# Kernel tuning notes

Hardware: AMD Instinct MI355X
Metric: run time of the kernel (lower is better)

The kernel has to match this reference:

```python
import jax, jax.numpy as jnp
import numpy as np

NUM_ENTITIES = 100000
BATCH_SIZE = 4096
E_STATIC = 250000
E_NEW = 4096
D_ENT = 128
D_REL = 64
N_REL = 9
N_TYPES = 3
N_INTENTS = 8
NUM_LAYERS = 3
SCALE = 0.05


def _make_edges(key, n):
    ks = jax.random.split(key, 5)
    src = jax.random.randint(ks[0], (n,), 0, NUM_ENTITIES, dtype=jnp.int32)
    st = jax.random.randint(ks[1], (n,), 0, N_TYPES, dtype=jnp.int32)
    tgt = jax.random.randint(ks[2], (n,), 0, NUM_ENTITIES, dtype=jnp.int32)
    tt = jax.random.randint(ks[3], (n,), 0, N_TYPES, dtype=jnp.int32)
    rel = jax.random.randint(ks[4], (n,), 0, N_REL, dtype=jnp.int32)
    return jnp.stack([src, st, tgt, tt, rel], axis=1)


def setup_inputs() -> dict:
    key = jax.random.key(0)
    ks = jax.random.split(key, 16)
    return {
        'new_edges': _make_edges(ks[0], E_NEW),
        'new_node_types': jax.random.randint(ks[1], (BATCH_SIZE,), 0, N_TYPES, dtype=jnp.int32),
        'static_edges': _make_edges(ks[2], E_STATIC),
        'entity_embeddings': SCALE * jax.random.normal(ks[3], (NUM_ENTITIES - BATCH_SIZE, D_ENT), jnp.float32),
        'default_emb': SCALE * jax.random.normal(ks[4], (N_TYPES, D_ENT), jnp.float32),
        'relation_emb': SCALE * jax.random.normal(ks[5], (N_REL, D_REL), jnp.float32),
        'W_rel': SCALE * jax.random.normal(ks[6], (N_REL, D_ENT, D_REL), jnp.float32),
        'b_rel': SCALE * jax.random.normal(ks[7], (N_REL, D_REL), jnp.float32),
        'W_msg': SCALE * jax.random.normal(ks[8], (N_REL, D_ENT, D_ENT), jnp.float32),
        'W_intent': SCALE * jax.random.normal(ks[9], (N_TYPES, D_ENT, N_INTENTS), jnp.float32),
        'b_intent': SCALE * jax.random.normal(ks[10], (N_TYPES, N_INTENTS), jnp.float32),
        'W_ibn': SCALE * jax.random.normal(ks[11], (N_TYPES, N_INTENTS, N_REL), jnp.float32),
        'b_ibn': SCALE * jax.random.normal(ks[12], (N_TYPES, N_REL), jnp.float32),
    }


def multi_dense(lookups, values, W, b=None, act=None):
    # Same math as tf.gather(W, lookups) followed by values @ w, but computed
    # against all D (<=9) weight slices then selected, to avoid materializing
    # a [E, d_in, d_out] gathered-weights tensor.
    out_all = jnp.einsum('ei,dio->edo', values, W)  # [E, D, d_out]
    out = jnp.take_along_axis(out_all, lookups[:, None, None], axis=1)[:, 0]
    if b is not None:
        out = out + b[lookups]
    return act(out) if act is not None else out


def reference(new_edges, new_node_types, static_edges, entity_embeddings,
              default_emb, relation_emb, W_rel, b_rel, W_msg,
              W_intent, b_intent, W_ibn, b_ibn):
    edges = jnp.concatenate([new_edges, static_edges], axis=0)  # [E, 5]
    sources = edges[:, 0]
    targets = edges[:, 2]
    target_types = edges[:, 3]
    relations = edges[:, 4]

    rel_e = relation_emb[relations]  # [E, D_REL]
    # first BATCH_SIZE entity slots come from type default embeddings
    ent = jnp.concatenate([default_emb[new_node_types], entity_embeddings], axis=0)  # [N, D_ENT]

    layer_edge_weights = []
    for _ in range(NUM_LAYERS):
        src = ent[sources]  # [E, D_ENT]
        tgt = ent[targets]  # [E, D_ENT]
        # per-target intent distribution and per-relation intent weights
        intents = multi_dense(target_types, tgt, W_intent, b_intent, jax.nn.softmax)  # [E, N_INTENTS]
        rel_w = multi_dense(target_types, intents, W_ibn, b_ibn, jax.nn.softmax)  # [E, N_REL]
        iw = jnp.take_along_axis(rel_w, relations[:, None], axis=1)[:, 0]  # [E]
        # per-relation transform of source embeddings
        src_rel = multi_dense(relations, src, W_rel, b_rel, jax.nn.selu)  # [E, D_REL]
        scores = jnp.einsum('er,er,e->e', src_rel, rel_e, iw)  # [E]
        exp_s = jnp.exp(scores)
        denom = jax.ops.segment_sum(exp_s, targets, num_segments=NUM_ENTITIES)  # [N]
        # tf.math.reciprocal_no_nan semantics
        safe = jnp.where(denom != 0, denom, 1.0)
        recip = jnp.where(denom != 0, 1.0 / safe, 0.0)
        dist = exp_s * recip[targets]  # scatter-softmax over incoming edges
        # inference: dropout is identity
        msg = dist[:, None] * multi_dense(relations, src, W_msg, None, None)  # [E, D_ENT]
        ent = jax.ops.segment_sum(msg, targets, num_segments=NUM_ENTITIES)  # [N, D_ENT]
        layer_edge_weights.append(dist)

    return ent, jnp.stack(layer_edge_weights)  # [N, D_ENT], [L, E]
```

## Files before the change

### kernel.cpp

```cpp
#include <hip/hip_runtime.h>
#include <cstddef>
#include <cstdint>

#define NE 100000
#define EN 4096
#define ET 254096
#define D 128
#define DR 64
#define NR 9
#define NT 3
#define NI 8
#define TE 256
#define TILES_X 28

using frag  = __attribute__((ext_vector_type(8))) short;
using f32x4 = __attribute__((ext_vector_type(4))) float;

__device__ __forceinline__ ushort f2b(float x) {
  union { float f; uint32_t u; } v; v.f = x;
  uint32_t r = v.u + 0x7FFFu + ((v.u >> 16) & 1u);
  return (ushort)(r >> 16);
}

__device__ __forceinline__ uint32_t cvtpk(float lo, float hi) {
  uint32_t r;
  asm("v_cvt_pk_bf16_f32 %0, %1, %2" : "=v"(r) : "v"(lo), "v"(hi));
  return r;
}

__device__ __forceinline__ frag lds_rd(const ushort* b, int row, int k) {
  const int ch = ((k >> 3) ^ (row & 7));
  return *(const frag*)(b + row * D + (ch << 3));
}
__device__ __forceinline__ void lds_wr(ushort* b, int row, int ch, frag v) {
  *(frag*)(b + row * D + ((ch ^ (row & 7)) << 3)) = v;
}
__device__ __forceinline__ void lds_wr2(ushort* b, int row, int k, uint32_t v) {
  const int ch = (k >> 3) ^ (row & 7);
  *(uint32_t*)(b + row * D + (ch << 3) + (k & 7)) = v;
}

__global__ void k_init(ushort* __restrict__ entb, const int* __restrict__ ntypes,
                       const float* __restrict__ def, const float* __restrict__ emb) {
  int i = blockIdx.x * blockDim.x + threadIdx.x;
  if (i >= NE * (D / 4)) return;
  int row = i >> 5, ch = i & 31;
  float4 v;
  if (row < EN) v = ((const float4*)(def + ntypes[row] * D))[ch];
  else v = ((const float4*)(emb + (size_t)(row - EN) * D))[ch];
  ushort4 h;
  h.x = f2b(v.x); h.y = f2b(v.y); h.z = f2b(v.z); h.w = f2b(v.w);
  ((ushort4*)entb)[i] = h;
}

__global__ void k_zero_cnt(int* cnt) { if (threadIdx.x < 48) cnt[threadIdx.x] = 0; }

__global__ __launch_bounds__(256) void k_hist2(const int* __restrict__ nedg,
                                               const int* __restrict__ sedg,
                                               int* __restrict__ cnt,
                                               int* __restrict__ thist) {
  __shared__ int h[NR];
  if (threadIdx.x < NR) h[threadIdx.x] = 0;
  __syncthreads();
  int e = blockIdx.x * 256 + threadIdx.x;
  if (e < ET) {
    const int* p = (e < EN) ? nedg + (size_t)e * 5 : sedg + (size_t)(e - EN) * 5;
    atomicAdd(&h[p[4]], 1);
    atomicAdd(&thist[p[2]], 1);
  }
  __syncthreads();
  if (threadIdx.x < NR && h[threadIdx.x]) atomicAdd(&cnt[threadIdx.x], h[threadIdx.x]);
}

__global__ void k_prefix(const int* __restrict__ cnt, int* __restrict__ base,
                         int* __restrict__ head) {
  if (threadIdx.x == 0) {
    int acc = 0;
    for (int r = 0; r < NR; r++) { base[r] = acc; head[r] = acc; acc += cnt[r]; }
  }
}

__global__ __launch_bounds__(256) void k_scan1(const int* __restrict__ hist,
                                               int* __restrict__ local_ex,
                                               int* __restrict__ bsum, int n) {
  __shared__ int s[256];
  int i = blockIdx.x * 256 + threadIdx.x;
  int v = (i < n) ? hist[i] : 0;
  s[threadIdx.x] = v;
  __syncthreads();
  for (int off = 1; off < 256; off <<= 1) {
    int t = (threadIdx.x >= off) ? s[threadIdx.x - off] : 0;
    __syncthreads();
    s[threadIdx.x] += t;
    __syncthreads();
  }
  if (i < n) local_ex[i] = s[threadIdx.x] - v;
  if (threadIdx.x == 255) bsum[blockIdx.x] = s[255];
}

__global__ __launch_bounds__(512) void k_scan2(int* __restrict__ bsum, int nb) {
  __shared__ int s[512];
  int v = (threadIdx.x < nb) ? bsum[threadIdx.x] : 0;
  s[threadIdx.x] = v;
  __syncthreads();
  for (int off = 1; off < 512; off <<= 1) {
    int t = (threadIdx.x >= off) ? s[threadIdx.x - off] : 0;
    __syncthreads();
    s[threadIdx.x] += t;
    __syncthreads();
  }
  if (threadIdx.x < nb) bsum[threadIdx.x] = s[threadIdx.x] - v;
}

__global__ void k_scan3(int* __restrict__ tgt_off, const int* __restrict__ bsum,
                        int* __restrict__ thead) {
  int i = blockIdx.x * 256 + threadIdx.x;
  if (i < NE) {
    int v = tgt_off[i] + bsum[i >> 8];
    tgt_off[i] = v;
    thead[i] = v;
  }
  if (i == 0) tgt_off[NE] = ET;
}

__global__ __launch_bounds__(256) void k_scatter3(const int* __restrict__ nedg,
                                                  const int* __restrict__ sedg,
                                                  int* __restrict__ head,
                                                  int* __restrict__ thead,
                                                  int* __restrict__ bucket,
                                                  int* __restrict__ tpos,
                                                  int* __restrict__ esorted) {
  __shared__ int h[NR], bb[NR];
  if (threadIdx.x < NR) h[threadIdx.x] = 0;
  __syncthreads();
  int e = blockIdx.x * 256 + threadIdx.x;
  int r = -1, pos = 0, t = 0;
  if (e < ET) {
    const int* p = (e < EN) ? nedg + (size_t)e * 5 : sedg + (size_t)(e - EN) * 5;
    r = p[4]; t = p[2];
    pos = atomicAdd(&h[r], 1);
  }
  __syncthreads();
  if (threadIdx.x < NR)
    bb[threadIdx.x] = h[threadIdx.x] ? atomicAdd(&head[threadIdx.x], h[threadIdx.x]) : 0;
  __syncthreads();
  if (r >= 0) {
    bucket[bb[r] + pos] = e;
    int pt = atomicAdd(&thead[t], 1);
    tpos[e] = pt;
    esorted[pt] = e;
  }
}

__global__ __launch_bounds__(1024) void k_iw(
    const ushort* __restrict__ entb,
    const float* __restrict__ W_int, const float* __restrict__ b_int,
    const float* __restrict__ W_ibn, const float* __restrict__ b_ibn,
    float* __restrict__ IW) {
  __shared__ ushort sE[TE * D];
  __shared__ ushort sWi[NT * 16 * D];
  __shared__ float sInt3[TE * 25];
  __shared__ float sbint[NT * NI], sWibn[NT * NI * NR], sbibn[NT * NR];

  const int tid = threadIdx.x;
  const int lane = tid & 63, wv = tid >> 6, g = lane >> 4, c = lane & 15;

  {
    float a[2], b[2];
#pragma unroll
    for (int j = 0; j < 2; j++) {
      int i = tid + j * 1024;
      if (i < NT * NI * (D / 2)) {
        int tt = i / (NI * D / 2), rem = i % (NI * D / 2), jj = rem / (D / 2), k2 = rem % (D / 2);
        const float* Wi = W_int + (size_t)tt * D * NI;
        a[j] = Wi[(2 * k2) * NI + jj]; b[j] = Wi[(2 * k2 + 1) * NI + jj];
      }
    }
#pragma unroll
    for (int j = 0; j < 2; j++) {
      int i = tid + j * 1024;
      if (i < NT * NI * (D / 2)) {
        int tt = i / (NI * D / 2), rem = i % (NI * D / 2), jj = rem / (D / 2), k2 = rem % (D / 2);
        lds_wr2(sWi, tt * 16 + jj, 2 * k2, cvtpk(a[j], b[j]));
      }
    }
  }
  for (int i = tid; i < NT * 8 * (D / 2); i += 1024) {
    int tt = i / (8 * D / 2), rem = i % (8 * D / 2), j = rem / (D / 2), k2 = rem % (D / 2);
    lds_wr2(sWi, tt * 16 + 8 + j, 2 * k2, 0u);
  }
  if (tid < NT * NI) sbint[tid] = b_int[tid];
  for (int i = tid; i < NT * NI * NR; i += 1024) sWibn[i] = W_ibn[i];
  if (tid < NT * NR) sbibn[tid] = b_ibn[tid];

  const int ebase = blockIdx.x * TE;
  const int nrow = min(TE, NE - ebase);
  {
    frag tmp[4];
#pragma unroll
    for (int j = 0; j < 4; j++) {
      int i = tid + j * 1024, row = i >> 4, ch = i & 15;
      tmp[j] = (row < nrow) ? ((const frag*)(entb + (size_t)(ebase + row) * D))[ch] : (frag){};
    }
#pragma unroll
    for (int j = 0; j < 4; j++) {
      int i = tid + j * 1024, row = i >> 4, ch = i & 15;
      lds_wr(sE, row, ch, tmp[j]);
    }
  }
  __syncthreads();

  {
    f32x4 accI[NT];
#pragma unroll
    for (int tt = 0; tt < NT; tt++) accI[tt] = (f32x4){0.f, 0.f, 0.f, 0.f};
#pragma unroll
    for (int ks = 0; ks < 4; ks++) {
      const int k = ks * 32 + g * 8;
      frag a = lds_rd(sE, wv * 16 + c, k);
#pragma unroll
      for (int tt = 0; tt < NT; tt++) {
        frag b = lds_rd(sWi, tt * 16 + c, k);
        accI[tt] = __builtin_amdgcn_mfma_f32_16x16x32_bf16(a, b, accI[tt], 0, 0, 0);
      }
    }
    if (c < NI) {
      const int rb = wv * 16 + g * 4;
#pragma unroll
      for (int tt = 0; tt < NT; tt++)
#pragma unroll
        for (int q = 0; q < 4; q++) sInt3[(rb + q) * 25 + tt * 8 + c] = accI[tt][q];
    }
  }
  __syncthreads();

  float* stg = (float*)sE;
  {
    const int row = tid & 255, tt = tid >> 8;
    if (tt < NT && row < nrow) {
      float it[NI], mx = -1e30f;
#pragma unroll
      for (int j = 0; j < NI; j++) {
        it[j] = sInt3[row * 25 + tt * 8 + j] + sbint[tt * NI + j];
        mx = fmaxf(mx, it[j]);
      }
      float ssum = 0.f;
#pragma unroll
      for (int j = 0; j < NI; j++) { it[j] = __expf(it[j] - mx); ssum += it[j]; }
      const float inv = 1.f / ssum;
      float qv[NR];
#pragma unroll
      for (int k = 0; k < NR; k++) qv[k] = sbibn[tt * NR + k];
#pragma unroll
      for (int j = 0; j < NI; j++) {
        const float ij = it[j] * inv;
#pragma unroll
        for (int k = 0; k < NR; k++) qv[k] = fmaf(ij, sWibn[(tt * NI + j) * NR + k], qv[k]);
      }
      float m9 = qv[0];
#pragma unroll
      for (int k = 1; k < NR; k++) m9 = fmaxf(m9, qv[k]);
      float s9 = 0.f;
#pragma unroll
      for (int k = 0; k < NR; k++) s9 += __expf(qv[k] - m9);
      const float i9 = 1.f / s9;
#pragma unroll
      for (int k = 0; k < NR; k++) stg[row * 27 + tt * 9 + k] = __expf(qv[k] - m9) * i9;
    }
  }
  __syncthreads();

  const int n27 = nrow * 27;
  float* outp = IW + (size_t)ebase * 27;
  for (int i = tid; i < n27; i += 1024) outp[i] = stg[i];
}

__global__ __launch_bounds__(1024) void k_pass1(
    const ushort* __restrict__ entb,
    const int* __restrict__ nedg, const int* __restrict__ sedg,
    const int* __restrict__ cnt, const int* __restrict__ base_g,
    const int* __restrict__ bucket, const int* __restrict__ tpos,
    const float* __restrict__ IW,
    const float* __restrict__ rel_emb,
    const float* __restrict__ W_rel, const float* __restrict__ b_rel,
    const float* __restrict__ W_msg,
    ushort* __restrict__ msgbuf, float* __restrict__ exps_s) {
  const int r = blockIdx.y;
  __shared__ ushort sA[TE * D];
  __shared__ ushort sWm[D * D];
  __shared__ ushort sWr[DR * D];
  __shared__ int sTP[TE];
  __shared__ float sIW[TE];
  __shared__ float sbrel[DR], srele[DR];

  const int tid = threadIdx.x;
  const int lane = tid & 63;
  const int wv = tid >> 6;
  const int g = lane >> 4;
  const int c = lane & 15;

  {
    const float* Wr = W_rel + (size_t)r * D * DR;
    const float* Wm = W_msg + (size_t)r * D * D;
    float ra[4], rb[4], ma[8], mb[8];
#pragma unroll
    for (int j = 0; j < 4; j++) {
      int i = tid + j * 1024, k2 = i / DR, n = i % DR;
      ra[j] = Wr[(2 * k2) * DR + n]; rb[j] = Wr[(2 * k2 + 1) * DR + n];
    }
#pragma unroll
    for (int j = 0; j < 8; j++) {
      int i = tid + j * 1024, k2 = i >> 7, n = i & 127;
      ma[j] = Wm[(2 * k2) * D + n]; mb[j] = Wm[(2 * k2 + 1) * D + n];
    }
#pragma unroll
    for (int j = 0; j < 4; j++) {
      int i = tid + j * 1024, k2 = i / DR, n = i % DR;
      lds_wr2(sWr, n, 2 * k2, cvtpk(ra[j], rb[j]));
    }
#pragma unroll
    for (int j = 0; j < 8; j++) {
      int i = tid + j * 1024, k2 = i >> 7, n = i & 127;
      lds_wr2(sWm, n, 2 * k2, cvtpk(ma[j], mb[j]));
    }
  }
  if (tid < DR) { sbrel[tid] = b_rel[r * DR + tid]; srele[tid] = rel_emb[r * DR + tid]; }

  const int nr = cnt[r];
  const int bbase = base_g[r];
  const int ntiles = (nr + TE - 1) / TE;

  for (int tile = blockIdx.x; tile < ntiles; tile += gridDim.x) {
    const int e0 = tile * TE;
    const int ne = min(TE, nr - e0);
    __syncthreads();

    {
      const int row = tid & 255, h = tid >> 8;
      int eg = 0;
      if (row < ne) eg = bucket[bbase + e0 + row];
      const int* p = (eg < EN) ? nedg + (size_t)eg * 5 : sedg + (size_t)(eg - EN) * 5;
      const int s = p[0];
      if (h == 0 && row < ne) {
        const int t = p[2], tt = p[3];
        sTP[row] = tpos[eg];
        sIW[row] = IW[((size_t)t * NT + tt) * NR + r];
      }
      const frag* rp = (const frag*)(entb + (size_t)s * D);
      frag tmp[4];
#pragma unroll
      for (int j = 0; j < 4; j++) tmp[j] = rp[h * 4 + j];
#pragma unroll
      for (int j = 0; j < 4; j++) lds_wr(sA, row, h * 4 + j, tmp[j]);
    }
    __syncthreads();

    f32x4 accR[4], accM[8];
#pragma unroll
    for (int nt = 0; nt < 4; nt++) accR[nt] = (f32x4){0.f, 0.f, 0.f, 0.f};
#pragma unroll
    for (int nt = 0; nt < 8; nt++) accM[nt] = (f32x4){0.f, 0.f, 0.f, 0.f};
#pragma unroll
    for (int ks = 0; ks < 4; ks++) {
      const int k = ks * 32 + g * 8;
      frag a0 = lds_rd(sA, wv * 16 + c, k);
#pragma unroll
      for (int nt = 0; nt < 4; nt++) {
        frag b = lds_rd(sWr, nt * 16 + c, k);
        accR[nt] = __builtin_amdgcn_mfma_f32_16x16x32_bf16(a0, b, accR[nt], 0, 0, 0);
      }
#pragma unroll
      for (int nt = 0; nt < 8; nt++) {
        frag b = lds_rd(sWm, nt * 16 + c, k);
        accM[nt] = __builtin_amdgcn_mfma_f32_16x16x32_bf16(a0, b, accM[nt], 0, 0, 0);
      }
    }

    const int mb = wv * 16 + g * 4;

    float es[4];
    {
      float v[4] = {0.f, 0.f, 0.f, 0.f};
#pragma unroll
      for (int nt = 0; nt < 4; nt++) {
        const int col = nt * 16 + c;
        const float br = sbrel[col], re = srele[col];
#pragma unroll
        for (int q = 0; q < 4; q++) {
          const float x = accR[nt][q] + br;
          const float sl = x > 0.f ? 1.0507009873554805f * x
                                   : 1.7580993408473766f * (__expf(x) - 1.f);
          v[q] = fmaf(sl, re, v[q]);
        }
      }
#pragma unroll
      for (int off = 1; off < 16; off <<= 1)
#pragma unroll
        for (int q = 0; q < 4; q++) v[q] += __shfl_xor(v[q], off, 64);
#pragma unroll
      for (int q = 0; q < 4; q++) {
        const int m = mb + q;
        es[q] = __expf(v[q] * sIW[m]);
        if (c == 0 && m < ne) exps_s[sTP[m]] = es[q];
      }
    }

    {
#pragma unroll
      for (int q = 0; q < 4; q++) {
        const int m = mb + q;
        ushort* mrow = msgbuf + (size_t)sTP[m] * D;
#pragma unroll
        for (int nt = 0; nt < 8; nt++) {
          float val = accM[nt][q] * es[q];
          float other = __shfl_xor(val, 1, 64);
          if (!(c & 1) && m < ne)
            *(uint32_t*)(mrow + nt * 16 + c) = cvtpk(val, other);
        }
      }
    }
  }
}

__global__ __launch_bounds__(256) void k_agg(
    const ushort* __restrict__ msgbuf, const float* __restrict__ exps_s,
    const int* __restrict__ tgt_off, const int* __restrict__ esorted,
    ushort* __restrict__ entb, float* __restrict__ fout,
    float* __restrict__ dout, int last) {
  const int lg = threadIdx.x & 15;
  const int grp = threadIdx.x >> 4;
  const int ngrp = gridDim.x * 16;
  for (int t = blockIdx.x * 16 + grp; t < NE; t += ngrp) {
    const int beg = tgt_off[t], end = tgt_off[t + 1];
    float a[8] = {0.f, 0.f, 0.f, 0.f, 0.f, 0.f, 0.f, 0.f};
    float dsum = 0.f;
    for (int j = beg; j < end; j++) {
      const uint4 pk = *(const uint4*)(msgbuf + (size_t)j * D + lg * 8);
      dsum += exps_s[j];
      a[0] += __uint_as_float(pk.x << 16); a[1] += __uint_as_float(pk.x & 0xFFFF0000u);
      a[2] += __uint_as_float(pk.y << 16); a[3] += __uint_as_float(pk.y & 0xFFFF0000u);
      a[4] += __uint_as_float(pk.z << 16); a[5] += __uint_as_float(pk.z & 0xFFFF0000u);
      a[6] += __uint_as_float(pk.w << 16); a[7] += __uint_as_float(pk.w & 0xFFFF0000u);
    }
    const float rec = (dsum != 0.f) ? 1.f / dsum : 0.f;
#pragma unroll
    for (int i = 0; i < 8; i++) a[i] *= rec;
    if (last) {
      float4* o = (float4*)(fout + (size_t)t * D + lg * 8);
      o[0] = make_float4(a[0], a[1], a[2], a[3]);
      o[1] = make_float4(a[4], a[5], a[6], a[7]);
    } else {
      uint4 pk;
      pk.x = (uint32_t)f2b(a[0]) | ((uint32_t)f2b(a[1]) << 16);
      pk.y = (uint32_t)f2b(a[2]) | ((uint32_t)f2b(a[3]) << 16);
      pk.z = (uint32_t)f2b(a[4]) | ((uint32_t)f2b(a[5]) << 16);
      pk.w = (uint32_t)f2b(a[6]) | ((uint32_t)f2b(a[7]) << 16);
      *(uint4*)(entb + (size_t)t * D + lg * 8) = pk;
    }
    for (int j = beg + lg; j < end; j += 16) dout[esorted[j]] = exps_s[j] * rec;
  }
}

extern "C" void kernel_launch(void* const* d_in, const int* in_sizes, int n_in,
                              void* d_out, int out_size, void* d_ws, size_t ws_size,
                              hipStream_t stream) {
  const int* nedg = (const int*)d_in[0];
  const int* ntypes = (const int*)d_in[1];
  const int* sedg = (const int*)d_in[2];
  const float* emb = (const float*)d_in[3];
  const float* def = (const float*)d_in[4];
  const float* rel_emb = (const float*)d_in[5];
  const float* W_rel = (const float*)d_in[6];
  const float* b_rel = (const float*)d_in[7];
  const float* W_msg = (const float*)d_in[8];
  const float* W_int = (const float*)d_in[9];
  const float* b_int = (const float*)d_in[10];
  const float* W_ibn = (const float*)d_in[11];
  const float* b_ibn = (const float*)d_in[12];
  float* out = (float*)d_out;

  char* w = (char*)d_ws;
  size_t off = 0;
  ushort* entb = (ushort*)(w + off); off += (size_t)NE * D * 2;
  ushort* msgbuf = (ushort*)(w + off); off += (size_t)ET * D * 2;
  float* exps_s = (float*)(w + off); off += (size_t)ET * 4;
  int* bucket = (int*)(w + off); off += (size_t)ET * 4;
  int* tpos = (int*)(w + off); off += (size_t)ET * 4;
  int* esorted = (int*)(w + off); off += (size_t)ET * 4;
  int* tgt_off = (int*)(w + off); off += (size_t)(NE + 4) * 4;
  int* thead = (int*)(w + off); off += (size_t)NE * 4;
  int* thist = (int*)(w + off); off += (size_t)NE * 4;
  int* bsum = (int*)(w + off); off += 2048;
  int* cnt = (int*)(w + off); off += 192;
  float* IW = (float*)(w + off); off += (size_t)NE * NT * NR * 4;
  int* base_g = cnt + 16;
  int* head = cnt + 32;
  float* dist_base = out + (size_t)NE * D;

  const int eblocks = (ET + 255) / 256;
  const int nb = (NE + 255) / 256;

  k_init<<<dim3((NE * (D / 4) + 255) / 256), 256, 0, stream>>>(entb, ntypes, def, emb);
  k_zero_cnt<<<1, 64, 0, stream>>>(cnt);
  hipMemsetAsync(thist, 0, (size_t)NE * 4, stream);
  k_hist2<<<dim3(eblocks), 256, 0, stream>>>(nedg, sedg, cnt, thist);
  k_prefix<<<1, 64, 0, stream>>>(cnt, base_g, head);
  k_scan1<<<dim3(nb), 256, 0, stream>>>(thist, tgt_off, bsum, NE);
  k_scan2<<<1, 512, 0, stream>>>(bsum, nb);
  k_scan3<<<dim3(nb), 256, 0, stream>>>(tgt_off, bsum, thead);
  k_scatter3<<<dim3(eblocks), 256, 0, stream>>>(nedg, sedg, head, thead, bucket, tpos,
                                                esorted);

  for (int l = 0; l < 3; l++) {
    k_iw<<<dim3(nb), 1024, 0, stream>>>(entb, W_int, b_int, W_ibn, b_ibn, IW);
    k_pass1<<<dim3(TILES_X, NR), 1024, 0, stream>>>(
        entb, nedg, sedg, cnt, base_g, bucket, tpos, IW, rel_emb, W_rel, b_rel, W_msg,
        msgbuf, exps_s);
    k_agg<<<dim3(2048), 256, 0, stream>>>(msgbuf, exps_s, tgt_off, esorted, entb, out,
                                          dist_base + (size_t)l * ET, l == 2);
  }
}
```

Baseline: 357.1 us.

## Halve pass1 edge tile, cache W_rel fragments in registers, run two blocks/CU

Shrinks the per-relation edge tile in k_pass1 from 256 to 128 rows and the block from 1024 to 512 threads, with launch bounds asking for two blocks per CU. The W_rel tile is staged through the sA buffer once and then held in registers as MFMA B fragments, which drops the sWr LDS array and its repeated LDS reads in the inner loop. The lower LDS footprint is meant to let two blocks share a CU, so one block's gather and load phases can overlap the other's MFMA work. The cost is more register pressure from the 16 cached fragments and a doubled tile count per relation. k_iw is changed to hard-code 256 rows so it keeps its old tiling.

```diff
diff --git a/kernel.cpp b/kernel.cpp
--- a/kernel.cpp
+++ b/kernel.cpp
@@ -10,8 +10,8 @@
 #define NR 9
 #define NT 3
 #define NI 8
-#define TE 256
-#define TILES_X 28
+#define TE 128
+#define TILES_X 56
 
 using frag  = __attribute__((ext_vector_type(8))) short;
 using f32x4 = __attribute__((ext_vector_type(4))) float;
@@ -157,9 +157,9 @@
     const float* __restrict__ W_int, const float* __restrict__ b_int,
     const float* __restrict__ W_ibn, const float* __restrict__ b_ibn,
     float* __restrict__ IW) {
-  __shared__ ushort sE[TE * D];
+  __shared__ ushort sE[256 * D];
   __shared__ ushort sWi[NT * 16 * D];
-  __shared__ float sInt3[TE * 25];
+  __shared__ float sInt3[256 * 25];
   __shared__ float sbint[NT * NI], sWibn[NT * NI * NR], sbibn[NT * NR];
 
   const int tid = threadIdx.x;
@@ -193,8 +193,8 @@
   for (int i = tid; i < NT * NI * NR; i += 1024) sWibn[i] = W_ibn[i];
   if (tid < NT * NR) sbibn[tid] = b_ibn[tid];
 
-  const int ebase = blockIdx.x * TE;
-  const int nrow = min(TE, NE - ebase);
+  const int ebase = blockIdx.x * 256;
+  const int nrow = min(256, NE - ebase);
   {
     frag tmp[4];
 #pragma unroll
@@ -275,7 +275,7 @@
   for (int i = tid; i < n27; i += 1024) outp[i] = stg[i];
 }
 
-__global__ __launch_bounds__(1024) void k_pass1(
+__global__ __launch_bounds__(512, 2) void k_pass1(
     const ushort* __restrict__ entb,
     const int* __restrict__ nedg, const int* __restrict__ sedg,
     const int* __restrict__ cnt, const int* __restrict__ base_g,
@@ -288,7 +288,6 @@
   const int r = blockIdx.y;
   __shared__ ushort sA[TE * D];
   __shared__ ushort sWm[D * D];
-  __shared__ ushort sWr[DR * D];
   __shared__ int sTP[TE];
   __shared__ float sIW[TE];
   __shared__ float sbrel[DR], srele[DR];
@@ -302,29 +301,24 @@
   {
     const float* Wr = W_rel + (size_t)r * D * DR;
     const float* Wm = W_msg + (size_t)r * D * D;
-    float ra[4], rb[4], ma[8], mb[8];
-#pragma unroll
-    for (int j = 0; j < 4; j++) {
-      int i = tid + j * 1024, k2 = i / DR, n = i % DR;
-      ra[j] = Wr[(2 * k2) * DR + n]; rb[j] = Wr[(2 * k2 + 1) * DR + n];
-    }
-#pragma unroll
-    for (int j = 0; j < 8; j++) {
-      int i = tid + j * 1024, k2 = i >> 7, n = i & 127;
-      ma[j] = Wm[(2 * k2) * D + n]; mb[j] = Wm[(2 * k2 + 1) * D + n];
-    }
-#pragma unroll
-    for (int j = 0; j < 4; j++) {
-      int i = tid + j * 1024, k2 = i / DR, n = i % DR;
-      lds_wr2(sWr, n, 2 * k2, cvtpk(ra[j], rb[j]));
-    }
-#pragma unroll
-    for (int j = 0; j < 8; j++) {
-      int i = tid + j * 1024, k2 = i >> 7, n = i & 127;
-      lds_wr2(sWm, n, 2 * k2, cvtpk(ma[j], mb[j]));
+    for (int i = tid; i < (D / 2) * DR; i += 512) {
+      int k2 = i / DR, n = i % DR;
+      lds_wr2(sA, n, 2 * k2, cvtpk(Wr[(2 * k2) * DR + n], Wr[(2 * k2 + 1) * DR + n]));
+    }
+    for (int i = tid; i < (D / 2) * D; i += 512) {
+      int k2 = i >> 7, n = i & 127;
+      lds_wr2(sWm, n, 2 * k2, cvtpk(Wm[(2 * k2) * D + n], Wm[(2 * k2 + 1) * D + n]));
     }
   }
   if (tid < DR) { sbrel[tid] = b_rel[r * DR + tid]; srele[tid] = rel_emb[r * DR + tid]; }
+  __syncthreads();
+
+  frag bR[4][4];
+#pragma unroll
+  for (int nt = 0; nt < 4; nt++)
+#pragma unroll
+    for (int ks = 0; ks < 4; ks++)
+      bR[nt][ks] = lds_rd(sA, nt * 16 + c, ks * 32 + g * 8);
 
   const int nr = cnt[r];
   const int bbase = base_g[r];
@@ -336,7 +330,7 @@
     __syncthreads();
 
     {
-      const int row = tid & 255, h = tid >> 8;
+      const int row = tid & 127, h = tid >> 7;
       int eg = 0;
       if (row < ne) eg = bucket[bbase + e0 + row];
       const int* p = (eg < EN) ? nedg + (size_t)eg * 5 : sedg + (size_t)(eg - EN) * 5;
@@ -365,10 +359,8 @@
       const int k = ks * 32 + g * 8;
       frag a0 = lds_rd(sA, wv * 16 + c, k);
 #pragma unroll
-      for (int nt = 0; nt < 4; nt++) {
-        frag b = lds_rd(sWr, nt * 16 + c, k);
-        accR[nt] = __builtin_amdgcn_mfma_f32_16x16x32_bf16(a0, b, accR[nt], 0, 0, 0);
-      }
+      for (int nt = 0; nt < 4; nt++)
+        accR[nt] = __builtin_amdgcn_mfma_f32_16x16x32_bf16(a0, bR[nt][ks], accR[nt], 0, 0, 0);
 #pragma unroll
       for (int nt = 0; nt < 8; nt++) {
         frag b = lds_rd(sWm, nt * 16 + c, k);
@@ -513,7 +505,7 @@
 
   for (int l = 0; l < 3; l++) {
     k_iw<<<dim3(nb), 1024, 0, stream>>>(entb, W_int, b_int, W_ibn, b_ibn, IW);
-    k_pass1<<<dim3(TILES_X, NR), 1024, 0, stream>>>(
+    k_pass1<<<dim3(TILES_X, NR), 512, 0, stream>>>(
         entb, nedg, sedg, cnt, base_g, bucket, tpos, IW, rel_emb, W_rel, b_rel, W_msg,
         msgbuf, exps_s);
     k_agg<<<dim3(2048), 256, 0, stream>>>(msgbuf, exps_s, tgt_off, esorted, entb, out,
```

After: 392.6 us. 10.0% more time.

## Pre-pack edge metadata, pre-convert weights to bf16, and prefetch next tile in pass1

Applied to the files above, without the earlier changes.

Edge metadata (source, IW row offset, target position) is packed into one int4 per relation-sorted edge during the scatter, replacing the bucket, edge-array and tpos lookups chained together in pass1. W_rel and W_msg are converted once to swizzled bf16 in a new kernel, so each pass1 block copies them straight into LDS instead of converting from fp32. Pass1 also software-prefetches the next tile's gathered rows and IW values into registers while the current tile computes. The costs are extra register pressure, a 16-byte-per-edge workspace, and one more launch.

```diff
diff --git a/kernel.cpp b/kernel.cpp
--- a/kernel.cpp
+++ b/kernel.cpp
@@ -55,6 +55,33 @@
 
 __global__ void k_zero_cnt(int* cnt) { if (threadIdx.x < 48) cnt[threadIdx.x] = 0; }
 
+__global__ __launch_bounds__(256) void k_wconv(const float* __restrict__ Wr,
+                                               const float* __restrict__ Wm,
+                                               ushort* __restrict__ wrelb,
+                                               ushort* __restrict__ wmsgb) {
+  const int nrel = NR * DR * (D / 8);
+  const int nmsg = NR * D * (D / 8);
+  int idx = blockIdx.x * 256 + threadIdx.x;
+  if (idx < nrel) {
+    int r = idx / (DR * 16), rem = idx % (DR * 16), n = rem / 16, sc = rem % 16;
+    int kb = (sc ^ (n & 7)) * 8;
+    const float* s = Wr + (size_t)r * D * DR + (size_t)kb * DR + n;
+    uint4 pk;
+    pk.x = cvtpk(s[0 * DR], s[1 * DR]); pk.y = cvtpk(s[2 * DR], s[3 * DR]);
+    pk.z = cvtpk(s[4 * DR], s[5 * DR]); pk.w = cvtpk(s[6 * DR], s[7 * DR]);
+    *(uint4*)(wrelb + (size_t)r * DR * D + n * D + sc * 8) = pk;
+  } else if (idx < nrel + nmsg) {
+    int j = idx - nrel;
+    int r = j / (D * 16), rem = j % (D * 16), n = rem / 16, sc = rem % 16;
+    int kb = (sc ^ (n & 7)) * 8;
+    const float* s = Wm + (size_t)r * D * D + (size_t)kb * D + n;
+    uint4 pk;
+    pk.x = cvtpk(s[0 * D], s[1 * D]); pk.y = cvtpk(s[2 * D], s[3 * D]);
+    pk.z = cvtpk(s[4 * D], s[5 * D]); pk.w = cvtpk(s[6 * D], s[7 * D]);
+    *(uint4*)(wmsgb + (size_t)r * D * D + n * D + sc * 8) = pk;
+  }
+}
+
 __global__ __launch_bounds__(256) void k_hist2(const int* __restrict__ nedg,
                                                const int* __restrict__ sedg,
                                                int* __restrict__ cnt,
@@ -127,17 +154,16 @@
                                                   const int* __restrict__ sedg,
                                                   int* __restrict__ head,
                                                   int* __restrict__ thead,
-                                                  int* __restrict__ bucket,
-                                                  int* __restrict__ tpos,
+                                                  int4* __restrict__ epack,
                                                   int* __restrict__ esorted) {
   __shared__ int h[NR], bb[NR];
   if (threadIdx.x < NR) h[threadIdx.x] = 0;
   __syncthreads();
   int e = blockIdx.x * 256 + threadIdx.x;
-  int r = -1, pos = 0, t = 0;
+  int r = -1, pos = 0, s = 0, t = 0, tt = 0;
   if (e < ET) {
     const int* p = (e < EN) ? nedg + (size_t)e * 5 : sedg + (size_t)(e - EN) * 5;
-    r = p[4]; t = p[2];
+    s = p[0]; t = p[2]; tt = p[3]; r = p[4];
     pos = atomicAdd(&h[r], 1);
   }
   __syncthreads();
@@ -145,9 +171,8 @@
     bb[threadIdx.x] = h[threadIdx.x] ? atomicAdd(&head[threadIdx.x], h[threadIdx.x]) : 0;
   __syncthreads();
   if (r >= 0) {
-    bucket[bb[r] + pos] = e;
     int pt = atomicAdd(&thead[t], 1);
-    tpos[e] = pt;
+    epack[bb[r] + pos] = make_int4(s, (t * NT + tt) * NR, pt, 0);
     esorted[pt] = e;
   }
 }
@@ -157,9 +182,9 @@
     const float* __restrict__ W_int, const float* __restrict__ b_int,
     const float* __restrict__ W_ibn, const float* __restrict__ b_ibn,
     float* __restrict__ IW) {
-  __shared__ ushort sE[TE * D];
+  __shared__ ushort sE[256 * D];
   __shared__ ushort sWi[NT * 16 * D];
-  __shared__ float sInt3[TE * 25];
+  __shared__ float sInt3[256 * 25];
   __shared__ float sbint[NT * NI], sWibn[NT * NI * NR], sbibn[NT * NR];
 
   const int tid = threadIdx.x;
@@ -193,8 +218,8 @@
   for (int i = tid; i < NT * NI * NR; i += 1024) sWibn[i] = W_ibn[i];
   if (tid < NT * NR) sbibn[tid] = b_ibn[tid];
 
-  const int ebase = blockIdx.x * TE;
-  const int nrow = min(TE, NE - ebase);
+  const int ebase = blockIdx.x * 256;
+  const int nrow = min(256, NE - ebase);
   {
     frag tmp[4];
 #pragma unroll
@@ -277,13 +302,11 @@
 
 __global__ __launch_bounds__(1024) void k_pass1(
     const ushort* __restrict__ entb,
-    const int* __restrict__ nedg, const int* __restrict__ sedg,
+    const int4* __restrict__ epack,
     const int* __restrict__ cnt, const int* __restrict__ base_g,
-    const int* __restrict__ bucket, const int* __restrict__ tpos,
     const float* __restrict__ IW,
-    const float* __restrict__ rel_emb,
-    const float* __restrict__ W_rel, const float* __restrict__ b_rel,
-    const float* __restrict__ W_msg,
+    const float* __restrict__ rel_emb, const float* __restrict__ b_rel,
+    const ushort* __restrict__ wrelb, const ushort* __restrict__ wmsgb,
     ushort* __restrict__ msgbuf, float* __restrict__ exps_s) {
   const int r = blockIdx.y;
   __shared__ ushort sA[TE * D];
@@ -298,31 +321,14 @@
   const int wv = tid >> 6;
   const int g = lane >> 4;
   const int c = lane & 15;
+  const int row = tid & 255, h = tid >> 8;
 
   {
-    const float* Wr = W_rel + (size_t)r * D * DR;
-    const float* Wm = W_msg + (size_t)r * D * D;
-    float ra[4], rb[4], ma[8], mb[8];
-#pragma unroll
-    for (int j = 0; j < 4; j++) {
-      int i = tid + j * 1024, k2 = i / DR, n = i % DR;
-      ra[j] = Wr[(2 * k2) * DR + n]; rb[j] = Wr[(2 * k2 + 1) * DR + n];
-    }
-#pragma unroll
-    for (int j = 0; j < 8; j++) {
-      int i = tid + j * 1024, k2 = i >> 7, n = i & 127;
-      ma[j] = Wm[(2 * k2) * D + n]; mb[j] = Wm[(2 * k2 + 1) * D + n];
-    }
-#pragma unroll
-    for (int j = 0; j < 4; j++) {
-      int i = tid + j * 1024, k2 = i / DR, n = i % DR;
-      lds_wr2(sWr, n, 2 * k2, cvtpk(ra[j], rb[j]));
-    }
-#pragma unroll
-    for (int j = 0; j < 8; j++) {
-      int i = tid + j * 1024, k2 = i >> 7, n = i & 127;
-      lds_wr2(sWm, n, 2 * k2, cvtpk(ma[j], mb[j]));
-    }
+    const frag* wr = (const frag*)(wrelb + (size_t)r * DR * D);
+    ((frag*)sWr)[tid] = wr[tid];
+    const frag* wm = (const frag*)(wmsgb + (size_t)r * D * D);
+    ((frag*)sWm)[tid] = wm[tid];
+    ((frag*)sWm)[tid + 1024] = wm[tid + 1024];
   }
   if (tid < DR) { sbrel[tid] = b_rel[r * DR + tid]; srele[tid] = rel_emb[r * DR + tid]; }
 
@@ -330,30 +336,31 @@
   const int bbase = base_g[r];
   const int ntiles = (nr + TE - 1) / TE;
 
-  for (int tile = blockIdx.x; tile < ntiles; tile += gridDim.x) {
-    const int e0 = tile * TE;
-    const int ne = min(TE, nr - e0);
+  int4 mp; frag tmp[4]; float iwv = 0.f;
+  auto prefetch = [&](int t_) {
+    int eidx = t_ * TE + row;
+    if (eidx >= nr) eidx = 0;
+    mp = epack[bbase + eidx];
+    const frag* rp = (const frag*)(entb + (size_t)mp.x * D);
+#pragma unroll
+    for (int j = 0; j < 4; j++) tmp[j] = rp[h * 4 + j];
+    iwv = IW[mp.y + r];
+  };
+
+  int tile = blockIdx.x;
+  if (tile < ntiles) prefetch(tile);
+
+  for (; tile < ntiles; tile += gridDim.x) {
+    const int ne = min(TE, nr - tile * TE);
     __syncthreads();
 
-    {
-      const int row = tid & 255, h = tid >> 8;
-      int eg = 0;
-      if (row < ne) eg = bucket[bbase + e0 + row];
-      const int* p = (eg < EN) ? nedg + (size_t)eg * 5 : sedg + (size_t)(eg - EN) * 5;
-      const int s = p[0];
-      if (h == 0 && row < ne) {
-        const int t = p[2], tt = p[3];
-        sTP[row] = tpos[eg];
-        sIW[row] = IW[((size_t)t * NT + tt) * NR + r];
-      }
-      const frag* rp = (const frag*)(entb + (size_t)s * D);
-      frag tmp[4];
-#pragma unroll
-      for (int j = 0; j < 4; j++) tmp[j] = rp[h * 4 + j];
-#pragma unroll
-      for (int j = 0; j < 4; j++) lds_wr(sA, row, h * 4 + j, tmp[j]);
-    }
+#pragma unroll
+    for (int j = 0; j < 4; j++) lds_wr(sA, row, h * 4 + j, tmp[j]);
+    if (h == 0) { sTP[row] = mp.z; sIW[row] = iwv; }
     __syncthreads();
+
+    const int nxt = tile + gridDim.x;
+    if (nxt < ntiles) prefetch(nxt);
 
     f32x4 accR[4], accM[8];
 #pragma unroll
@@ -484,8 +491,7 @@
   ushort* entb = (ushort*)(w + off); off += (size_t)NE * D * 2;
   ushort* msgbuf = (ushort*)(w + off); off += (size_t)ET * D * 2;
   float* exps_s = (float*)(w + off); off += (size_t)ET * 4;
-  int* bucket = (int*)(w + off); off += (size_t)ET * 4;
-  int* tpos = (int*)(w + off); off += (size_t)ET * 4;
+  int4* epack = (int4*)(w + off); off += (size_t)ET * 16;
   int* esorted = (int*)(w + off); off += (size_t)ET * 4;
   int* tgt_off = (int*)(w + off); off += (size_t)(NE + 4) * 4;
   int* thead = (int*)(w + off); off += (size_t)NE * 4;
@@ -493,29 +499,31 @@
   int* bsum = (int*)(w + off); off += 2048;
   int* cnt = (int*)(w + off); off += 192;
   float* IW = (float*)(w + off); off += (size_t)NE * NT * NR * 4;
+  ushort* wrelb = (ushort*)(w + off); off += (size_t)NR * DR * D * 2;
+  ushort* wmsgb = (ushort*)(w + off); off += (size_t)NR * D * D * 2;
   int* base_g = cnt + 16;
   int* head = cnt + 32;
   float* dist_base = out + (size_t)NE * D;
 
   const int eblocks = (ET + 255) / 256;
   const int nb = (NE + 255) / 256;
+  const int wblocks = (NR * DR * (D / 8) + NR * D * (D / 8) + 255) / 256;
 
   k_init<<<dim3((NE * (D / 4) + 255) / 256), 256, 0, stream>>>(entb, ntypes, def, emb);
   k_zero_cnt<<<1, 64, 0, stream>>>(cnt);
   hipMemsetAsync(thist, 0, (size_t)NE * 4, stream);
+  k_wconv<<<dim3(wblocks), 256, 0, stream>>>(W_rel, W_msg, wrelb, wmsgb);
   k_hist2<<<dim3(eblocks), 256, 0, stream>>>(nedg, sedg, cnt, thist);
   k_prefix<<<1, 64, 0, stream>>>(cnt, base_g, head);
   k_scan1<<<dim3(nb), 256, 0, stream>>>(thist, tgt_off, bsum, NE);
   k_scan2<<<1, 512, 0, stream>>>(bsum, nb);
   k_scan3<<<dim3(nb), 256, 0, stream>>>(tgt_off, bsum, thead);
-  k_scatter3<<<dim3(eblocks), 256, 0, stream>>>(nedg, sedg, head, thead, bucket, tpos,
-                                                esorted);
+  k_scatter3<<<dim3(eblocks), 256, 0, stream>>>(nedg, sedg, head, thead, epack, esorted);
 
   for (int l = 0; l < 3; l++) {
     k_iw<<<dim3(nb), 1024, 0, stream>>>(entb, W_int, b_int, W_ibn, b_ibn, IW);
     k_pass1<<<dim3(TILES_X, NR), 1024, 0, stream>>>(
-        entb, nedg, sedg, cnt, base_g, bucket, tpos, IW, rel_emb, W_rel, b_rel, W_msg,
-        msgbuf, exps_s);
+        entb, epack, cnt, base_g, IW, rel_emb, b_rel, wrelb, wmsgb, msgbuf, exps_s);
     k_agg<<<dim3(2048), 256, 0, stream>>>(msgbuf, exps_s, tgt_off, esorted, entb, out,
                                           dist_base + (size_t)l * ET, l == 2);
   }
```

Result: faster. 340.1 us (-4.8%).
